# Kernel tuning notes

Measured on AMD Instinct MI355X. Metric: run time of the kernel, lower is better.

Reference implementation:

```python
import jax, jax.numpy as jnp
import numpy as np

B = 32; NMAX = 256; E = 512; H = 512; U = 256; M = 32; L = 2; P = 4; TAU = 1.0
S = NMAX + 1                      # pseudo-seq len = nodes + SOS
IN0 = E + (M - 1) + P             # GRU layer-0 input size


def setup_inputs() -> dict:
    key = jax.random.key(0)
    ks = jax.random.split(key, 22)
    f = lambda k, sh, sc=0.05: jax.random.normal(k, sh, dtype=jnp.float32) * sc
    return {
        "h_padded": jax.random.normal(ks[0], (B, NMAX, E), jnp.float32),
        "hg": jax.random.normal(ks[1], (B, E), jnp.float32),
        "num_nodes": jax.random.randint(ks[2], (B,), 1, NMAX + 1),
        "u_noise": jax.random.uniform(ks[3], (M, B, S), jnp.float32),
        "emb_special": f(ks[4], (2, E), 1.0),
        "emb_pos": f(ks[5], (M, P), 1.0),
        "Wp": f(ks[6], (L * H, E)), "bp": f(ks[7], (L * H,)),
        "W_ih0": f(ks[8], (3 * H, IN0)), "W_hh0": f(ks[9], (3 * H, H)),
        "b_ih0": f(ks[10], (3 * H,)), "b_hh0": f(ks[11], (3 * H,)),
        "W_ih1": f(ks[12], (3 * H, H)), "W_hh1": f(ks[13], (3 * H, H)),
        "b_ih1": f(ks[14], (3 * H,)), "b_hh1": f(ks[15], (3 * H,)),
        "W1": f(ks[16], (U, H)), "W2": f(ks[17], (U, H)),
        "wc": f(ks[18], (U,)), "V": f(ks[19], (U,)),
        "Wf": f(ks[20], (M - 1, H)), "bf": f(ks[21], (M - 1,)),
    }


def _gru_step(x, hid, params):
    # torch nn.GRU single time step, L layers; gate order (r, z, n)
    new = []
    inp = x
    for l, (Wi, Wh, bi, bh) in enumerate(params):
        hp = hid[l]
        gi = inp @ Wi.T + bi
        gh = hp @ Wh.T + bh
        gi_r, gi_z, gi_n = jnp.split(gi, 3, axis=-1)
        gh_r, gh_z, gh_n = jnp.split(gh, 3, axis=-1)
        r = jax.nn.sigmoid(gi_r + gh_r)
        z = jax.nn.sigmoid(gi_z + gh_z)
        n = jnp.tanh(gi_n + r * gh_n)
        hn = (1.0 - z) * n + z * hp
        new.append(hn)
        inp = hn
    return inp, jnp.stack(new, 0)


def reference(h_padded, hg, num_nodes, u_noise, emb_special, emb_pos, Wp, bp,
              W_ih0, W_hh0, b_ih0, b_hh0, W_ih1, W_hh1, b_ih1, b_hh1,
              W1, W2, wc, V, Wf, bf):
    lens = num_nodes + 1
    mask = jnp.arange(S)[None, :] < lens[:, None]                       # [B,S]
    node_valid = (jnp.arange(NMAX)[None, :] < num_nodes[:, None]).astype(h_padded.dtype)
    # encoder_out = [SOS emb ; h nodes ; zero pad] as pad_sequence would give
    sos_enc = jnp.broadcast_to(emb_special[1], (B, 1, E))
    encoder_out = jnp.concatenate([sos_enc, h_padded * node_valid[..., None]], axis=1)  # [B,S,E]
    enc_W1 = encoder_out @ W1.T                                          # [B,S,U] hoisted (loop-invariant)
    dec_hidden = jnp.tanh(hg @ Wp.T + bp).reshape(B, L, H).transpose(1, 0, 2)  # [L,B,H]
    theta0 = jnp.zeros((B, M - 1), encoder_out.dtype)
    dec_input = jnp.concatenate([jnp.broadcast_to(emb_special[0], (B, E)), theta0], axis=1)
    cov_vec0 = jnp.zeros((B, S), encoder_out.dtype)
    gumbel = -jnp.log(-jnp.log(u_noise + 1e-10) + 1e-10)                 # [M,B,S]
    gru_params = ((W_ih0, W_hh0, b_ih0, b_hh0), (W_ih1, W_hh1, b_ih1, b_hh1))
    neg = jnp.float32(-1e30)

    def step(carry, xs):
        dec_in, hid, cov_vec, cov_loss = carry
        i, pe, g = xs
        x = jnp.concatenate([dec_in, jnp.broadcast_to(pe, (B, P))], axis=1)
        out, hid = _gru_step(x, hid, gru_params)                        # out [B,H]
        # Bahdanau attention with coverage
        uj = enc_W1 + (out @ W2.T)[:, None, :] + cov_vec[..., None] * wc
        uj = jnp.tanh(uj) @ V                                           # [B,S]
        aj = jax.nn.softmax(jnp.where(mask, uj, neg), axis=-1)
        # hard gumbel-softmax (straight-through)
        logits = jnp.log(aj + 1e-12)
        y = jax.nn.softmax((logits + g) / TAU, axis=1)
        onehot = jax.nn.one_hot(jnp.argmax(y, axis=1), S, dtype=y.dtype)
        hard = jax.lax.stop_gradient(onehot - y) + y
        chosen = jnp.einsum('bse,bs->be', encoder_out, hard)            # [B,E]
        cov_loss = cov_loss + jnp.minimum(aj, cov_vec).sum()
        cov_vec = cov_vec + aj
        theta = jnp.where(i < 1,
                          jnp.zeros((B, M - 1), out.dtype),
                          jax.nn.sigmoid(out @ Wf.T + bf))
        dec_next = jnp.concatenate([chosen, theta], axis=1)
        return (dec_next, hid, cov_vec, cov_loss), (hard, theta, aj)

    init = (dec_input, dec_hidden, cov_vec0, jnp.float32(0.0))
    xs = (jnp.arange(M), emb_pos, gumbel)
    carry_f, (hards, thetas, ajs) = jax.lax.scan(step, init, xs)
    cov_loss = carry_f[3] / B
    pointer = jnp.transpose(hards, (1, 2, 0))   # [B,S,M]
    adj = jnp.transpose(thetas, (1, 2, 0))      # [B,M-1,M]
    atts = jnp.transpose(ajs, (1, 2, 0))        # [B,S,M]
    return pointer, cov_loss, encoder_out, adj, atts
```

## Files before the change

kernel.cpp:

```cpp
#include <hip/hip_runtime.h>

constexpr int NB  = 32;
constexpr int NMX = 256;
constexpr int ED  = 512;
constexpr int HD  = 512;
constexpr int UD  = 256;
constexpr int MS  = 32;
constexpr int PD  = 4;
constexpr int SD  = 257;
constexpr int IL0 = 547;
constexpr int XP  = 576;

constexpr long long OFF_PTR  = 0;
constexpr long long OFF_COVL = (long long)NB*SD*MS;
constexpr long long OFF_ENC  = OFF_COVL + 1;
constexpr long long OFF_ADJ  = OFF_ENC + (long long)NB*SD*ED;
constexpr long long OFF_ATT  = OFF_ADJ + (long long)NB*(MS-1)*MS;

__device__ __forceinline__ float sigf(float x){ return 1.0f/(1.0f + __expf(-x)); }
__device__ __forceinline__ float ftanh(float x){ float e = __expf(2.0f*x); return 1.0f - 2.0f/(e + 1.0f); }

__global__ __launch_bounds__(256) void k_init(const float* __restrict__ hp,
                      const float* __restrict__ embsp, const float* __restrict__ embpos,
                      const float* __restrict__ W1, const float* __restrict__ Wih0,
                      const float* __restrict__ W2, const int* __restrict__ nn,
                      float* __restrict__ out, float* __restrict__ x4,
                      float* __restrict__ cov, float* __restrict__ covl,
                      float* __restrict__ W1T, float* __restrict__ Wih0_4,
                      float* __restrict__ W2T){
  int blk = blockIdx.x, t = threadIdx.x;
  {
    int r = blk*2 + (t >> 7);
    int tid = t & 127;
    int b = r / SD, s = r % SD;
    float* dst = out + OFF_ENC + (long long)r*ED + tid*4;
    if (s == 0){
      const float* src = embsp + ED + tid*4;
      dst[0] = src[0]; dst[1] = src[1]; dst[2] = src[2]; dst[3] = src[3];
    } else if (s-1 < nn[b]){
      const float* src = hp + ((long long)b*NMX + (s-1))*ED + tid*4;
      float4 v = *(const float4*)src;
      dst[0] = v.x; dst[1] = v.y; dst[2] = v.z; dst[3] = v.w;
    } else {
      dst[0] = 0.f; dst[1] = 0.f; dst[2] = 0.f; dst[3] = 0.f;
    }
  }
  const int N0 = XP*NB;
  const int N1 = N0 + NB*SD;
  const int N2 = N1 + NB;
  const int N3 = N2 + UD*ED;
  const int N4 = N3 + 1536*XP;
  const int N5 = N4 + ED*UD;
  for (int i = blk*256 + t; i < N5; i += 4112*256){
    if (i < N0){
      int kb = i >> 7, r = i & 3;
      int k = kb*4 + r;
      float v;
      if (k < ED) v = embsp[k];
      else if (k < ED + MS - 1) v = 0.f;
      else if (k < IL0) v = embpos[k - (ED + MS - 1)];
      else v = 0.f;
      x4[i] = v;
    } else if (i < N1){
      cov[i - N0] = 0.f;
    } else if (i < N2){
      covl[i - N1] = 0.f;
    } else if (i < N3){
      int j = i - N2; int k = j / UD, u = j % UD;
      W1T[j] = W1[(long long)u*ED + k];
    } else if (i < N4){
      int j = i - N3; int row = j / XP, c = j % XP;
      Wih0_4[j] = (c < IL0) ? Wih0[(long long)row*IL0 + c] : 0.f;
    } else {
      int j = i - N4; int k = j / UD, u = j % UD;
      W2T[j] = W2[(long long)u*HD + k];
    }
  }
}

__global__ __launch_bounds__(256) void k_ew1h(const float* __restrict__ out,
                        const float4* __restrict__ W1T4, float4* __restrict__ encW1,
                        const int* __restrict__ nn,
                        const float* __restrict__ hg, const float4* __restrict__ Wp4,
                        const float* __restrict__ bp, float* __restrict__ h0,
                        float* __restrict__ h1){
  __shared__ __align__(16) float As[16][68];
  __shared__ __align__(16) float Bs[16][68];
  int blk = blockIdx.x, t = threadIdx.x;
  if (blk < 516){
    int bm = blk >> 2, bn = blk & 3;
    int m0 = bm*64, n0 = bn*64;
    {
      int rr = m0 + (t & 63);
      bool act = false;
      if (rr < NB*SD){
        int b = rr / SD, s = rr % SD;
        act = (s <= nn[b]);
      }
      if (!__any(act)) return;
    }
    const float* A = out + OFF_ENC;
    int tm = t >> 4, tn = t & 15;
    float4 acc[4];
    #pragma unroll
    for (int i = 0; i < 4; ++i) acc[i] = {0.f,0.f,0.f,0.f};
    int arow = t >> 2, akq = t & 3;
    int bk = t >> 4, bnq = t & 15;
    for (int k0 = 0; k0 < 512; k0 += 16){
      float av[4];
      bool okA = (m0 + arow) < NB*SD;
      long long abase = (long long)(m0 + arow)*ED + k0 + akq*4;
      #pragma unroll
      for (int j = 0; j < 4; ++j) av[j] = okA ? A[abase + j] : 0.f;
      float4 bv = W1T4[(long long)(k0 + bk)*64 + (n0 >> 2) + bnq];
      __syncthreads();
      #pragma unroll
      for (int j = 0; j < 4; ++j) As[akq*4 + j][arow] = av[j];
      *(float4*)&Bs[bk][bnq*4] = bv;
      __syncthreads();
      #pragma unroll
      for (int kk = 0; kk < 16; ++kk){
        float4 a = *(const float4*)&As[kk][tm*4];
        float4 bq = *(const float4*)&Bs[kk][tn*4];
        acc[0].x += a.x*bq.x; acc[0].y += a.x*bq.y; acc[0].z += a.x*bq.z; acc[0].w += a.x*bq.w;
        acc[1].x += a.y*bq.x; acc[1].y += a.y*bq.y; acc[1].z += a.y*bq.z; acc[1].w += a.y*bq.w;
        acc[2].x += a.z*bq.x; acc[2].y += a.z*bq.y; acc[2].z += a.z*bq.z; acc[2].w += a.z*bq.w;
        acc[3].x += a.w*bq.x; acc[3].y += a.w*bq.y; acc[3].z += a.w*bq.z; acc[3].w += a.w*bq.w;
      }
    }
    #pragma unroll
    for (int i = 0; i < 4; ++i){
      int r = m0 + tm*4 + i;
      if (r < NB*SD) encW1[(long long)r*64 + (n0 >> 2) + tn] = acc[i];
    }
  } else {
    int b = t & 31;
    int row = (blk - 516)*8 + (t >> 5);
    const float4* w = Wp4 + (long long)row*128;
    const float4* xg = (const float4*)(hg + (long long)b*ED);
    float acc = bp[row];
    #pragma unroll 4
    for (int i = 0; i < 128; ++i){
      float4 wv = w[i], xv = xg[i];
      acc += wv.x*xv.x + wv.y*xv.y + wv.z*xv.z + wv.w*xv.w;
    }
    float v = ftanh(acc);
    int h = row & 511;
    int idx = (h >> 2)*128 + b*4 + (h & 3);
    if (row < HD) h0[idx] = v;
    else          h1[idx] = v;
  }
}

template<int PER>
__global__ __launch_bounds__(512) void k_gru(const float4* __restrict__ x4,
                      const float4* __restrict__ h4,
                      const float4* __restrict__ Wih4, const float4* __restrict__ Whh4,
                      const float* __restrict__ bih, const float* __restrict__ bhh,
                      float* __restrict__ outT){
  constexpr int NI4 = PER*8;
  __shared__ float part[2][NB][8][6];
  int t = threadIdx.x;
  int b = t & 31, ks = (t >> 5) & 7, hl = (t >> 8) & 1;
  int h = blockIdx.x*2 + hl;
  float ai0 = 0.f, ai1 = 0.f, ai2 = 0.f, ah0 = 0.f, ah1 = 0.f, ah2 = 0.f;
  {
    const float4* w0 = Wih4 + (long long)(0*HD + h)*NI4 + ks*PER;
    const float4* w1 = Wih4 + (long long)(1*HD + h)*NI4 + ks*PER;
    const float4* w2 = Wih4 + (long long)(2*HD + h)*NI4 + ks*PER;
    const float4* xb = x4 + (long long)(ks*PER)*NB + b;
    #pragma unroll
    for (int kb = 0; kb < PER; ++kb){
      float4 xv = xb[kb*NB];
      float4 a = w0[kb], c = w1[kb], d = w2[kb];
      ai0 += xv.x*a.x + xv.y*a.y + xv.z*a.z + xv.w*a.w;
      ai1 += xv.x*c.x + xv.y*c.y + xv.z*c.z + xv.w*c.w;
      ai2 += xv.x*d.x + xv.y*d.y + xv.z*d.z + xv.w*d.w;
    }
  }
  {
    const float4* w0 = Whh4 + (long long)(0*HD + h)*128 + ks*16;
    const float4* w1 = Whh4 + (long long)(1*HD + h)*128 + ks*16;
    const float4* w2 = Whh4 + (long long)(2*HD + h)*128 + ks*16;
    const float4* hb = h4 + (long long)(ks*16)*NB + b;
    #pragma unroll
    for (int kb = 0; kb < 16; ++kb){
      float4 xv = hb[kb*NB];
      float4 a = w0[kb], c = w1[kb], d = w2[kb];
      ah0 += xv.x*a.x + xv.y*a.y + xv.z*a.z + xv.w*a.w;
      ah1 += xv.x*c.x + xv.y*c.y + xv.z*c.z + xv.w*c.w;
      ah2 += xv.x*d.x + xv.y*d.y + xv.z*d.z + xv.w*d.w;
    }
  }
  part[hl][b][ks][0] = ai0; part[hl][b][ks][1] = ai1; part[hl][b][ks][2] = ai2;
  part[hl][b][ks][3] = ah0; part[hl][b][ks][4] = ah1; part[hl][b][ks][5] = ah2;
  __syncthreads();
  if (t < 64){
    int b2 = t & 31, hl2 = t >> 5;
    int h2 = blockIdx.x*2 + hl2;
    float g0=0.f,g1=0.f,g2=0.f,g3=0.f,g4=0.f,g5=0.f;
    #pragma unroll
    for (int k = 0; k < 8; ++k){
      g0 += part[hl2][b2][k][0]; g1 += part[hl2][b2][k][1]; g2 += part[hl2][b2][k][2];
      g3 += part[hl2][b2][k][3]; g4 += part[hl2][b2][k][4]; g5 += part[hl2][b2][k][5];
    }
    float gir = g0 + bih[h2], giz = g1 + bih[HD + h2], gin = g2 + bih[2*HD + h2];
    float ghr = g3 + bhh[h2], ghz = g4 + bhh[HD + h2], ghn = g5 + bhh[2*HD + h2];
    float r = sigf(gir + ghr);
    float z = sigf(giz + ghz);
    float nn = ftanh(gin + r*ghn);
    int idx = (h2 >> 2)*128 + b2*4 + (h2 & 3);
    float hp = ((const float*)h4)[idx];
    outT[idx] = (1.f - z)*nn + z*hp;
  }
}

__global__ __launch_bounds__(512) void k_qs(const float4* __restrict__ h1,
                      const float4* __restrict__ W2T4, const float4* __restrict__ Wf4,
                      const float* __restrict__ bfv, const float* __restrict__ embpos,
                      int m, const float4* __restrict__ encW1,
                      const float4* __restrict__ wc4, const float4* __restrict__ V4,
                      const int* __restrict__ nn,
                      const float* __restrict__ cov, float* __restrict__ sc,
                      float* __restrict__ x4, float* __restrict__ out){
  __shared__ __align__(16) float h1s[512];
  __shared__ __align__(16) float wcs[256];
  __shared__ __align__(16) float Vs[256];
  __shared__ __align__(16) float qs[256];
  __shared__ __align__(16) float4 qpart[8][64];
  int t = threadIdx.x;
  int b = blockIdx.x >> 3, seg = blockIdx.x & 7;
  int n = nn[b];
  if (seg != 0 && seg*33 > n) return;
  if (t < 128) ((float4*)h1s)[t] = h1[t*NB + b];
  else if (t < 192) ((float4*)wcs)[t - 128] = wc4[t - 128];
  else if (t < 256) ((float4*)Vs)[t - 192] = V4[t - 192];
  __syncthreads();
  {
    int u4 = t & 63, kq = t >> 6;
    float4 acc = {0.f,0.f,0.f,0.f};
    const float4* w = W2T4 + (long long)(kq*64)*64 + u4;
    const float* hh = h1s + kq*64;
    #pragma unroll 4
    for (int k = 0; k < 64; ++k){
      float a = hh[k];
      float4 wv = w[(long long)k*64];
      acc.x += a*wv.x; acc.y += a*wv.y; acc.z += a*wv.z; acc.w += a*wv.w;
    }
    qpart[kq][u4] = acc;
  }
  __syncthreads();
  if (t < 64){
    float4 s = qpart[0][t];
    #pragma unroll
    for (int k = 1; k < 8; ++k){
      float4 p = qpart[k][t];
      s.x += p.x; s.y += p.y; s.z += p.z; s.w += p.w;
    }
    ((float4*)qs)[t] = s;
  } else if (seg == 0){
    int w = (t >> 6) - 1;
    int lane = t & 63;
    for (int j = w; j < MS-1; j += 7){
      const float4* wf = Wf4 + (long long)j*128 + lane*2;
      float4 w0 = wf[0], w1v = wf[1];
      const float4* hh4 = (const float4*)h1s + lane*2;
      float4 hv0 = hh4[0], hv1 = hh4[1];
      float d = w0.x*hv0.x + w0.y*hv0.y + w0.z*hv0.z + w0.w*hv0.w
              + w1v.x*hv1.x + w1v.y*hv1.y + w1v.z*hv1.z + w1v.w*hv1.w;
      for (int off = 32; off; off >>= 1) d += __shfl_xor(d, off);
      if (lane == 0){
        float th = (m < 1) ? 0.f : sigf(d + bfv[j]);
        out[OFF_ADJ + (long long)b*(MS-1)*MS + (long long)j*MS + m] = th;
        int k = ED + j;
        x4[(k >> 2)*128 + b*4 + (k & 3)] = th;
      }
    }
  }
  if (seg == 0 && t == 0 && m + 1 < MS){
    #pragma unroll
    for (int p = 0; p < PD; ++p){
      int k = ED + MS - 1 + p;
      x4[(k >> 2)*128 + b*4 + (k & 3)] = embpos[(m+1)*PD + p];
    }
  }
  __syncthreads();
  int lane = t & 63, wav = t >> 6;
  int s0 = seg*33;
  float4 q4 = ((const float4*)qs)[lane];
  float4 wv = ((const float4*)wcs)[lane];
  float4 vv = ((const float4*)Vs)[lane];
  for (int s = s0 + wav; s < s0 + 33 && s < SD; s += 8){
    if (s > n) continue;
    float cv = cov[b*SD + s];
    float4 e4 = encW1[((long long)b*SD + s)*64 + lane];
    float acc = vv.x*ftanh(e4.x + q4.x + cv*wv.x)
              + vv.y*ftanh(e4.y + q4.y + cv*wv.y)
              + vv.z*ftanh(e4.z + q4.z + cv*wv.z)
              + vv.w*ftanh(e4.w + q4.w + cv*wv.w);
    for (int off = 32; off; off >>= 1) acc += __shfl_xor(acc, off);
    if (lane == 0) sc[b*SD + s] = acc;
  }
}

__global__ __launch_bounds__(512) void k_soft(const float* __restrict__ sc,
                      const int* __restrict__ nn, const float* __restrict__ un, int m,
                      float* __restrict__ cov, float* __restrict__ covl,
                      float* __restrict__ out, float4* __restrict__ x4,
                      const float* __restrict__ enc){
  __shared__ float red[8]; __shared__ float redc[8]; __shared__ int redi[8];
  __shared__ float s_mx, s_den; __shared__ int s_k;
  int b = blockIdx.x, t = threadIdx.x;
  int lane = t & 63, wav = t >> 6;
  int n = nn[b];
  float sv = (t < SD) ? sc[b*SD + t] : -3.4e38f;
  float cv = (t < SD) ? cov[b*SD + t] : 0.f;
  float v1 = (t < SD && t <= n) ? sv : -3.4e38f;
  for (int off = 32; off; off >>= 1) v1 = fmaxf(v1, __shfl_xor(v1, off));
  if (lane == 0) red[wav] = v1;
  __syncthreads();
  if (t == 0){
    float mm = red[0];
    for (int i = 1; i < 8; ++i) mm = fmaxf(mm, red[i]);
    s_mx = mm;
  }
  __syncthreads();
  float ev = (t < SD && t <= n) ? __expf(sv - s_mx) : 0.f;
  float v2 = ev;
  for (int off = 32; off; off >>= 1) v2 += __shfl_xor(v2, off);
  if (lane == 0) red[wav] = v2;
  __syncthreads();
  if (t == 0){
    float ss = 0.f;
    for (int i = 0; i < 8; ++i) ss += red[i];
    s_den = ss;
  }
  __syncthreads();
  float aj = (t < SD) ? ev / s_den : 0.f;
  float yl = -3.4e38f; int idx = SD; float lcl = 0.f;
  if (t < SD){
    float u = un[((long long)m*NB + b)*SD + t];
    float g = -__logf(-__logf(u + 1e-10f) + 1e-10f);
    yl = __logf(aj + 1e-12f) + g;
    idx = t;
    lcl = fminf(aj, cv);
    cov[b*SD + t] = cv + aj;
    out[OFF_ATT + ((long long)b*SD + t)*MS + m] = aj;
  }
  for (int off = 32; off; off >>= 1){
    float oy = __shfl_xor(yl, off); int oi = __shfl_xor(idx, off);
    if (oy > yl || (oy == yl && oi < idx)){ yl = oy; idx = oi; }
  }
  for (int off = 32; off; off >>= 1) lcl += __shfl_xor(lcl, off);
  if (lane == 0){ red[wav] = yl; redi[wav] = idx; redc[wav] = lcl; }
  __syncthreads();
  if (t == 0){
    float by = red[0]; int bi = redi[0]; float cl = redc[0];
    for (int w = 1; w < 8; ++w){
      if (red[w] > by || (red[w] == by && redi[w] < bi)){ by = red[w]; bi = redi[w]; }
      cl += redc[w];
    }
    s_k = bi;
    covl[b] += cl;
  }
  __syncthreads();
  int kk = s_k;
  if (t < SD) out[OFF_PTR + ((long long)b*SD + t)*MS + m] = (t == kk) ? 1.f : 0.f;
  const float* er = enc + ((long long)b*SD + kk)*ED;
  if (t < 128){
    float4 v; v.x = er[t*4]; v.y = er[t*4+1]; v.z = er[t*4+2]; v.w = er[t*4+3];
    x4[t*NB + b] = v;
  }
}

__global__ void k_fin(const float* __restrict__ covl, float* __restrict__ out){
  if (threadIdx.x == 0 && blockIdx.x == 0){
    float s = 0.f;
    for (int i = 0; i < NB; ++i) s += covl[i];
    out[OFF_COVL] = s / (float)NB;
  }
}

extern "C" void kernel_launch(void* const* d_in, const int* in_sizes, int n_in,
                              void* d_out, int out_size, void* d_ws, size_t ws_size,
                              hipStream_t stream){
  const float* h_padded    = (const float*)d_in[0];
  const float* hg          = (const float*)d_in[1];
  const int*   num_nodes   = (const int*)  d_in[2];
  const float* u_noise     = (const float*)d_in[3];
  const float* emb_special = (const float*)d_in[4];
  const float* emb_pos     = (const float*)d_in[5];
  const float* Wp          = (const float*)d_in[6];
  const float* bp          = (const float*)d_in[7];
  const float* W_ih0       = (const float*)d_in[8];
  const float* W_hh0       = (const float*)d_in[9];
  const float* b_ih0       = (const float*)d_in[10];
  const float* b_hh0       = (const float*)d_in[11];
  const float* W_ih1       = (const float*)d_in[12];
  const float* W_hh1       = (const float*)d_in[13];
  const float* b_ih1       = (const float*)d_in[14];
  const float* b_hh1       = (const float*)d_in[15];
  const float* W1          = (const float*)d_in[16];
  const float* W2          = (const float*)d_in[17];
  const float* wc          = (const float*)d_in[18];
  const float* V           = (const float*)d_in[19];
  const float* Wf          = (const float*)d_in[20];
  const float* bf          = (const float*)d_in[21];
  float* out = (float*)d_out;

  float* ws      = (float*)d_ws;
  float* encW1   = ws;  ws += (long long)NB*SD*UD;
  float* Wih0_4  = ws;  ws += (long long)1536*XP;
  float* W1T     = ws;  ws += (long long)UD*ED;
  float* W2T     = ws;  ws += (long long)UD*ED;
  float* x4      = ws;  ws += XP*NB;
  float* h0      = ws;  ws += 2*HD*NB;
  float* h1      = ws;  ws += 2*HD*NB;
  float* cov     = ws;  ws += NB*SD;
  float* covl    = ws;  ws += NB;
  float* sc      = ws;  ws += NB*SD;

  k_init<<<4112, 256, 0, stream>>>(h_padded, emb_special, emb_pos, W1, W_ih0, W2,
                                   num_nodes, out, x4, cov, covl, W1T, Wih0_4, W2T);
  k_ew1h<<<644, 256, 0, stream>>>(out, (const float4*)W1T, (float4*)encW1,
                                  num_nodes, hg, (const float4*)Wp, bp, h0, h1);

  for (int m = 0; m < MS; ++m){
    float* h0c = h0 + (m & 1)*HD*NB;
    float* h0n = h0 + ((m + 1) & 1)*HD*NB;
    float* h1c = h1 + (m & 1)*HD*NB;
    float* h1n = h1 + ((m + 1) & 1)*HD*NB;
    k_gru<18><<<256, 512, 0, stream>>>((const float4*)x4, (const float4*)h0c,
        (const float4*)Wih0_4, (const float4*)W_hh0, b_ih0, b_hh0, h0n);
    k_gru<16><<<256, 512, 0, stream>>>((const float4*)h0n, (const float4*)h1c,
        (const float4*)W_ih1, (const float4*)W_hh1, b_ih1, b_hh1, h1n);
    k_qs  <<<256, 512, 0, stream>>>((const float4*)h1n, (const float4*)W2T,
        (const float4*)Wf, bf, emb_pos, m, (const float4*)encW1,
        (const float4*)wc, (const float4*)V, num_nodes, cov, sc, x4, out);
    k_soft<<<NB, 512, 0, stream>>>(sc, num_nodes, u_noise, m, cov, covl, out,
        (float4*)x4, out + OFF_ENC);
  }
  k_fin<<<1, 64, 0, stream>>>(covl, out);
}
```

Baseline: 1.290 ms.

## Transpose hg for coalesced Wp GEMV, drop GEMM early-exit, halve k_qs blocks

Adds a transposed copy of hg built in k_init so the Wp projection in k_ew1h reads hg coalesced across batch lanes. It also removes the early-exit that skipped encW1 GEMM tiles with only padded rows. k_qs now launches 4 segments of 65 positions per batch instead of 8 of 33. Fewer k_qs blocks means the per-block query/theta prologue runs fewer times, but each block scores more positions serially. Removing the skip makes the GEMM always compute padded rows.

```diff
diff --git a/kernel.cpp b/kernel.cpp
--- a/kernel.cpp
+++ b/kernel.cpp
@@ -21,10 +21,12 @@
 __device__ __forceinline__ float ftanh(float x){ float e = __expf(2.0f*x); return 1.0f - 2.0f/(e + 1.0f); }
 
 __global__ __launch_bounds__(256) void k_init(const float* __restrict__ hp,
+                      const float* __restrict__ hg,
                       const float* __restrict__ embsp, const float* __restrict__ embpos,
                       const float* __restrict__ W1, const float* __restrict__ Wih0,
                       const float* __restrict__ W2, const int* __restrict__ nn,
                       float* __restrict__ out, float* __restrict__ x4,
+                      float* __restrict__ hg4,
                       float* __restrict__ cov, float* __restrict__ covl,
                       float* __restrict__ W1T, float* __restrict__ Wih0_4,
                       float* __restrict__ W2T){
@@ -46,12 +48,13 @@
     }
   }
   const int N0 = XP*NB;
-  const int N1 = N0 + NB*SD;
-  const int N2 = N1 + NB;
-  const int N3 = N2 + UD*ED;
-  const int N4 = N3 + 1536*XP;
-  const int N5 = N4 + ED*UD;
-  for (int i = blk*256 + t; i < N5; i += 4112*256){
+  const int N1 = N0 + ED*NB;
+  const int N2 = N1 + NB*SD;
+  const int N3 = N2 + NB;
+  const int N4 = N3 + UD*ED;
+  const int N5 = N4 + 1536*XP;
+  const int N6 = N5 + ED*UD;
+  for (int i = blk*256 + t; i < N6; i += 4112*256){
     if (i < N0){
       int kb = i >> 7, r = i & 3;
       int k = kb*4 + r;
@@ -62,17 +65,21 @@
       else v = 0.f;
       x4[i] = v;
     } else if (i < N1){
-      cov[i - N0] = 0.f;
+      int j = i - N0;
+      int kb = j >> 7, b = (j >> 2) & 31, r = j & 3;
+      hg4[j] = hg[(long long)b*ED + kb*4 + r];
     } else if (i < N2){
-      covl[i - N1] = 0.f;
+      cov[i - N1] = 0.f;
     } else if (i < N3){
-      int j = i - N2; int k = j / UD, u = j % UD;
+      covl[i - N2] = 0.f;
+    } else if (i < N4){
+      int j = i - N3; int k = j / UD, u = j % UD;
       W1T[j] = W1[(long long)u*ED + k];
-    } else if (i < N4){
-      int j = i - N3; int row = j / XP, c = j % XP;
+    } else if (i < N5){
+      int j = i - N4; int row = j / XP, c = j % XP;
       Wih0_4[j] = (c < IL0) ? Wih0[(long long)row*IL0 + c] : 0.f;
     } else {
-      int j = i - N4; int k = j / UD, u = j % UD;
+      int j = i - N5; int k = j / UD, u = j % UD;
       W2T[j] = W2[(long long)u*HD + k];
     }
   }
@@ -80,8 +87,7 @@
 
 __global__ __launch_bounds__(256) void k_ew1h(const float* __restrict__ out,
                         const float4* __restrict__ W1T4, float4* __restrict__ encW1,
-                        const int* __restrict__ nn,
-                        const float* __restrict__ hg, const float4* __restrict__ Wp4,
+                        const float4* __restrict__ hg4, const float4* __restrict__ Wp4,
                         const float* __restrict__ bp, float* __restrict__ h0,
                         float* __restrict__ h1){
   __shared__ __align__(16) float As[16][68];
@@ -90,15 +96,6 @@
   if (blk < 516){
     int bm = blk >> 2, bn = blk & 3;
     int m0 = bm*64, n0 = bn*64;
-    {
-      int rr = m0 + (t & 63);
-      bool act = false;
-      if (rr < NB*SD){
-        int b = rr / SD, s = rr % SD;
-        act = (s <= nn[b]);
-      }
-      if (!__any(act)) return;
-    }
     const float* A = out + OFF_ENC;
     int tm = t >> 4, tn = t & 15;
     float4 acc[4];
@@ -137,11 +134,10 @@
     int b = t & 31;
     int row = (blk - 516)*8 + (t >> 5);
     const float4* w = Wp4 + (long long)row*128;
-    const float4* xg = (const float4*)(hg + (long long)b*ED);
     float acc = bp[row];
     #pragma unroll 4
     for (int i = 0; i < 128; ++i){
-      float4 wv = w[i], xv = xg[i];
+      float4 wv = w[i], xv = hg4[i*NB + b];
       acc += wv.x*xv.x + wv.y*xv.y + wv.z*xv.z + wv.w*xv.w;
     }
     float v = ftanh(acc);
@@ -229,9 +225,9 @@
   __shared__ __align__(16) float qs[256];
   __shared__ __align__(16) float4 qpart[8][64];
   int t = threadIdx.x;
-  int b = blockIdx.x >> 3, seg = blockIdx.x & 7;
+  int b = blockIdx.x >> 2, seg = blockIdx.x & 3;
   int n = nn[b];
-  if (seg != 0 && seg*33 > n) return;
+  if (seg != 0 && seg*65 > n) return;
   if (t < 128) ((float4*)h1s)[t] = h1[t*NB + b];
   else if (t < 192) ((float4*)wcs)[t - 128] = wc4[t - 128];
   else if (t < 256) ((float4*)Vs)[t - 192] = V4[t - 192];
@@ -286,11 +282,11 @@
   }
   __syncthreads();
   int lane = t & 63, wav = t >> 6;
-  int s0 = seg*33;
+  int s0 = seg*65;
   float4 q4 = ((const float4*)qs)[lane];
   float4 wv = ((const float4*)wcs)[lane];
   float4 vv = ((const float4*)Vs)[lane];
-  for (int s = s0 + wav; s < s0 + 33 && s < SD; s += 8){
+  for (int s = s0 + wav; s < s0 + 65 && s < SD; s += 8){
     if (s > n) continue;
     float cv = cov[b*SD + s];
     float4 e4 = encW1[((long long)b*SD + s)*64 + lane];
@@ -414,16 +410,17 @@
   float* W1T     = ws;  ws += (long long)UD*ED;
   float* W2T     = ws;  ws += (long long)UD*ED;
   float* x4      = ws;  ws += XP*NB;
+  float* hg4     = ws;  ws += ED*NB;
   float* h0      = ws;  ws += 2*HD*NB;
   float* h1      = ws;  ws += 2*HD*NB;
   float* cov     = ws;  ws += NB*SD;
   float* covl    = ws;  ws += NB;
   float* sc      = ws;  ws += NB*SD;
 
-  k_init<<<4112, 256, 0, stream>>>(h_padded, emb_special, emb_pos, W1, W_ih0, W2,
-                                   num_nodes, out, x4, cov, covl, W1T, Wih0_4, W2T);
+  k_init<<<4112, 256, 0, stream>>>(h_padded, hg, emb_special, emb_pos, W1, W_ih0, W2,
+                                   num_nodes, out, x4, hg4, cov, covl, W1T, Wih0_4, W2T);
   k_ew1h<<<644, 256, 0, stream>>>(out, (const float4*)W1T, (float4*)encW1,
-                                  num_nodes, hg, (const float4*)Wp, bp, h0, h1);
+                                  (const float4*)hg4, (const float4*)Wp, bp, h0, h1);
 
   for (int m = 0; m < MS; ++m){
     float* h0c = h0 + (m & 1)*HD*NB;
@@ -434,7 +431,7 @@
         (const float4*)Wih0_4, (const float4*)W_hh0, b_ih0, b_hh0, h0n);
     k_gru<16><<<256, 512, 0, stream>>>((const float4*)h0n, (const float4*)h1c,
         (const float4*)W_ih1, (const float4*)W_hh1, b_ih1, b_hh1, h1n);
-    k_qs  <<<256, 512, 0, stream>>>((const float4*)h1n, (const float4*)W2T,
+    k_qs  <<<128, 512, 0, stream>>>((const float4*)h1n, (const float4*)W2T,
         (const float4*)Wf, bf, emb_pos, m, (const float4*)encW1,
         (const float4*)wc, (const float4*)V, num_nodes, cov, sc, x4, out);
     k_soft<<<NB, 512, 0, stream>>>(sc, num_nodes, u_noise, m, cov, covl, out,
```

Result: slower. 1.378 ms (+6.9%).
